# Performance work log

Hardware: AMD Instinct MI355X
Metric: run time of the kernel (lower is better)

The kernel has to match this reference:

```python
import jax, jax.numpy as jnp
import numpy as np

D = 128; H = 4; DK = D // H; ZN = 64; V = 8

def _silu(x):
    return x * jax.nn.sigmoid(x)

def _mlp3(x, w1, b1, w2, b2, w3, b3):
    h = _silu(x @ w1 + b1)
    h = _silu(h @ w2 + b2)
    return h @ w3 + b3

def _snorm(x):
    # StaticLayerNorm: center, divide by unbiased std (torch .std default ddof=1)
    c = x - jnp.mean(x, axis=-1, keepdims=True)
    std = jnp.sqrt(jnp.sum(c * c, axis=-1, keepdims=True) / (x.shape[-1] - 1))
    std = jnp.where(std == 0, 1.0, std)
    return c / std

def setup_inputs():
    key = jax.random.key(0)
    ks = list(jax.random.split(key, 40)); ki = iter(ks)
    xs = (6.0 / (DK + D)) ** 0.5
    inp = {}
    inp["latent"] = jax.random.normal(next(ki), (ZN, D, V, V, V), jnp.float32)
    inp["nodes"] = jax.random.normal(next(ki), (ZN, D), jnp.float32)
    inp["t"] = jax.random.uniform(next(ki), (ZN,), jnp.float32)
    for nm in ("qw", "kw", "vw"):
        inp[nm] = jax.random.uniform(next(ki), (H, D, DK), jnp.float32, -xs, xs)
    for nm in ("qb", "kb", "vb"):
        inp[nm] = jnp.zeros((H, DK), jnp.float32)
    inp["ow"] = jax.random.normal(next(ki), (D, D), jnp.float32) * (1.0 / D) ** 0.5
    for pre, dout in (("an_gb", 2 * D), ("an_a", D), ("fn_gb", 2 * D), ("fn_a", D)):
        inp[pre + "_w1"] = jax.random.normal(next(ki), (D, D), jnp.float32) * 0.05
        inp[pre + "_b1"] = jnp.zeros((D,), jnp.float32)
        inp[pre + "_w2"] = jax.random.normal(next(ki), (D, D), jnp.float32) * 0.05
        inp[pre + "_b2"] = jnp.zeros((D,), jnp.float32)
        inp[pre + "_w3"] = jax.random.normal(next(ki), (D, dout), jnp.float32) * 0.05
        inp[pre + "_b3"] = jnp.zeros((dout,), jnp.float32)
    return inp

def reference(latent, nodes, t, qw, kw, vw, qb, kb, vb, ow,
              an_gb_w1, an_gb_b1, an_gb_w2, an_gb_b2, an_gb_w3, an_gb_b3,
              an_a_w1, an_a_b1, an_a_w2, an_a_b2, an_a_w3, an_a_b3,
              fn_gb_w1, fn_gb_b1, fn_gb_w2, fn_gb_b2, fn_gb_w3, fn_gb_b3,
              fn_a_w1, fn_a_b1, fn_a_w2, fn_a_b2, fn_a_w3, fn_a_b3):
    b, d, vx, vy, vz = latent.shape
    n = vx * vy * vz
    x = latent.reshape(b, d, n).transpose(0, 2, 1)  # [b, n, d]
    cond = nodes[:, None, :] + t[:, None, None]     # [b, 1, d]
    gb1 = _mlp3(cond, an_gb_w1, an_gb_b1, an_gb_w2, an_gb_b2, an_gb_w3, an_gb_b3)
    g1, be1 = jnp.split(gb1, 2, axis=-1)
    al1 = _mlp3(cond, an_a_w1, an_a_b1, an_a_w2, an_a_b2, an_a_w3, an_a_b3)
    gb2 = _mlp3(cond, fn_gb_w1, fn_gb_b1, fn_gb_w2, fn_gb_b2, fn_gb_w3, fn_gb_b3)
    g2, be2 = jnp.split(gb2, 2, axis=-1)
    al2 = _mlp3(cond, fn_a_w1, fn_a_b1, fn_a_w2, fn_a_b2, fn_a_w3, fn_a_b3)
    # FAITHFUL BUG REPRO: source unpacks adaLN's (gamma, beta, alpha) as (alpha, gamma, beta)
    alpha1, gamma1, beta1 = g1, be1, al1
    alpha2, gamma2, beta2 = g2, be2, al2
    x2 = gamma1 * _snorm(x) + beta1
    dk = d // qw.shape[0]
    Q = jnp.einsum('bnd,hdk->bhnk', x2, qw) + qb[None, :, None, :]
    K = jnp.einsum('bnd,hdk->bhnk', x2, kw) + kb[None, :, None, :]
    Vv = jnp.einsum('bnd,hdk->bhnk', x2, vw) + vb[None, :, None, :]
    S = jnp.einsum('bhnk,bhmk->bhnm', Q, K) / (dk ** 0.5)
    P = jax.nn.softmax(S, axis=-1)
    O = jnp.einsum('bhnm,bhmk->bhnk', P, Vv)
    O = O.transpose(0, 2, 3, 1).reshape(b, n, d)  # matches torch permute(0,2,3,1).reshape
    attn = O @ ow
    x = x + alpha1 * attn
    x2 = gamma2 * _snorm(x) + beta2
    x = x + alpha2 * x2  # NOTE: source forward never applies self.ffn (dead module)
    return x.transpose(0, 2, 1).reshape(b, d, vx, vy, vz)
```

## Files before the change

### kernel.cpp

```cpp
#include <hip/hip_runtime.h>
#include <hip/hip_bf16.h>
#include <math.h>


#define NB 64

typedef __attribute__((ext_vector_type(8))) short bf16x8;
typedef __attribute__((ext_vector_type(4))) float f32x4;

__device__ __forceinline__ float silu_f(float x) { return x / (1.0f + __expf(-x)); }
__device__ __forceinline__ unsigned short f2bf(float x) {
    __hip_bfloat16 h = __float2bfloat16(x);
    return *reinterpret_cast<unsigned short*>(&h);
}

__global__ void __launch_bounds__(256) k_prep(
    const float* __restrict__ qw, const float* __restrict__ kw,
    const float* __restrict__ vw, const float* __restrict__ ow,
    unsigned short* __restrict__ cT, unsigned short* __restrict__ owT)
{
    int idx = blockIdx.x*256 + threadIdx.x;
    if (idx < 49152) {
        int ph = idx >> 14, r = idx & 16383, c = r >> 7, d = r & 127;
        int h = c >> 5, kk = c & 31;
        const float* wp = ph==0 ? qw : (ph==1 ? kw : vw);
        cT[idx] = f2bf(wp[h*4096 + d*32 + kk]);
    } else {
        int r = idx - 49152, c = r >> 7, i = r & 127;
        owT[r] = f2bf(ow[i*128 + c]);
    }
}

__global__ void __launch_bounds__(128) k_cond(
    const float* __restrict__ nodes, const float* __restrict__ tv,
    const float* __restrict__ w10, const float* __restrict__ b10,
    const float* __restrict__ w20, const float* __restrict__ b20,
    const float* __restrict__ w30, const float* __restrict__ b30,
    const float* __restrict__ w11, const float* __restrict__ b11,
    const float* __restrict__ w21, const float* __restrict__ b21,
    const float* __restrict__ w31, const float* __restrict__ b31,
    const float* __restrict__ w12, const float* __restrict__ b12,
    const float* __restrict__ w22, const float* __restrict__ b22,
    const float* __restrict__ w32, const float* __restrict__ b32,
    const float* __restrict__ w13, const float* __restrict__ b13,
    const float* __restrict__ w23, const float* __restrict__ b23,
    const float* __restrict__ w33, const float* __restrict__ b33,
    float* __restrict__ mods)
{
    int blk = blockIdx.x;
    int b = blk >> 2, m = blk & 3;
    const float* W1 = m==0?w10 : m==1?w11 : m==2?w12 : w13;
    const float* B1 = m==0?b10 : m==1?b11 : m==2?b12 : b13;
    const float* W2 = m==0?w20 : m==1?w21 : m==2?w22 : w23;
    const float* B2 = m==0?b20 : m==1?b21 : m==2?b22 : b23;
    const float* W3 = m==0?w30 : m==1?w31 : m==2?w32 : w33;
    const float* B3 = m==0?b30 : m==1?b31 : m==2?b32 : b33;
    int dout256 = (m == 0 || m == 2);
    int slot = (m==0)?0 : (m==1)?2 : (m==2)?3 : 5;

    __shared__ float xs[128], h1[128], h2[128];
    int t = threadIdx.x;
    xs[t] = nodes[b*128 + t] + tv[b];
    __syncthreads();

    float acc = B1[t];
    for (int i = 0; i < 128; i++) acc += xs[i] * W1[i*128 + t];
    h1[t] = silu_f(acc);
    __syncthreads();

    acc = B2[t];
    for (int i = 0; i < 128; i++) acc += h1[i] * W2[i*128 + t];
    h2[t] = silu_f(acc);
    __syncthreads();

    if (dout256) {
        float a0 = B3[t], a1 = B3[t + 128];
        for (int i = 0; i < 128; i++) {
            float h = h2[i];
            a0 += h * W3[i*256 + t];
            a1 += h * W3[i*256 + t + 128];
        }
        mods[((size_t)b*6 + slot    )*128 + t] = a0;
        mods[((size_t)b*6 + slot + 1)*128 + t] = a1;
    } else {
        float a0 = B3[t];
        for (int i = 0; i < 128; i++) a0 += h2[i] * W3[i*128 + t];
        mods[((size_t)b*6 + slot)*128 + t] = a0;
    }
}

__global__ void __launch_bounds__(256, 4) k_norm_qkv(
    const float* __restrict__ latent, const float* __restrict__ mods,
    const unsigned short* __restrict__ cT,
    const float* __restrict__ qb, const float* __restrict__ kb, const float* __restrict__ vb,
    unsigned short* __restrict__ Qb, unsigned short* __restrict__ Kb,
    unsigned short* __restrict__ Vtb)
{
    __shared__ unsigned short xb[64*136];

    int blk = blockIdx.x;
    int b = blk >> 3, n0 = (blk & 7) * 64;
    int t = threadIdx.x;
    int j = t >> 2, sub = t & 3;

    const float* lp = latent + (size_t)b*65536 + n0 + j;
    float lat[32];
    #pragma unroll
    for (int i = 0; i < 32; i++)
        lat[i] = lp[(size_t)(sub*32 + i)*512];

    float s = 0.f, ss = 0.f;
    #pragma unroll
    for (int i = 0; i < 32; i++) { s += lat[i]; ss += lat[i]*lat[i]; }
    s += __shfl_xor(s, 1); ss += __shfl_xor(ss, 1);
    s += __shfl_xor(s, 2); ss += __shfl_xor(ss, 2);
    float mean = s * (1.0f/128.0f);
    float var = (ss - 128.0f*mean*mean) * (1.0f/127.0f);
    var = var < 0.f ? 0.f : var;
    float sd = sqrtf(var);
    float rstd = (sd == 0.f) ? 1.f : 1.f/sd;

    const float* g1p  = mods + ((size_t)b*6 + 1)*128 + sub*32;
    const float* be1p = mods + ((size_t)b*6 + 2)*128 + sub*32;
    unsigned int* xbw = (unsigned int*)xb + j*68 + sub*16;
    #pragma unroll
    for (int i2 = 0; i2 < 16; i2++) {
        float v0 = g1p[2*i2]   * ((lat[2*i2]   - mean)*rstd) + be1p[2*i2];
        float v1 = g1p[2*i2+1] * ((lat[2*i2+1] - mean)*rstd) + be1p[2*i2+1];
        xbw[i2] = (unsigned)f2bf(v0) | ((unsigned)f2bf(v1) << 16);
    }
    __syncthreads();

    int w = t >> 6, lane = t & 63, lo = lane & 15, hi = lane >> 4;
    bf16x8 af[4];
    #pragma unroll
    for (int kc = 0; kc < 4; kc++)
        af[kc] = *(const bf16x8*)(xb + (w*16 + lo)*136 + kc*32 + hi*8);
    __syncthreads();

    const f32x4 zero = {0.f, 0.f, 0.f, 0.f};
    const float qscale = 0.17677669529663687f * 1.4426950408889634f;

    #pragma unroll 1
    for (int ph = 0; ph < 3; ph++) {
        const unsigned short* ct = cT + ph*16384;
        for (int nt = 0; nt < 8; nt++) {
            f32x4 acc = zero;
            #pragma unroll
            for (int kc = 0; kc < 4; kc++) {
                bf16x8 bf = *(const bf16x8*)(ct + (nt*16 + lo)*128 + kc*32 + hi*8);
                acc = __builtin_amdgcn_mfma_f32_16x16x32_bf16(af[kc], bf, acc, 0, 0, 0);
            }
            int c = nt*16 + lo, h = c >> 5, kk = c & 31;
            size_t bh = (size_t)(b*4 + h);
            if (ph == 0) {
                float bias = qb[c];
                #pragma unroll
                for (int jj = 0; jj < 4; jj++) {
                    int n = n0 + w*16 + hi*4 + jj;
                    Qb[(bh*512 + n)*32 + kk] = f2bf((acc[jj] + bias) * qscale);
                }
            } else if (ph == 1) {
                float bias = kb[c];
                #pragma unroll
                for (int jj = 0; jj < 4; jj++) {
                    int n = n0 + w*16 + hi*4 + jj;
                    Kb[(bh*512 + n)*32 + kk] = f2bf(acc[jj] + bias);
                }
            } else {
                float bias = vb[c];
                #pragma unroll
                for (int jj = 0; jj < 4; jj++) {
                    int nl = w*16 + hi*4 + jj;
                    xb[c*68 + nl] = f2bf(acc[jj] + bias);
                }
            }
        }
    }
    __syncthreads();
    for (int idx = t; idx < 8192; idx += 256) {
        int c = idx >> 6, jj = idx & 63;
        int h = c >> 5, kk = c & 31;
        size_t bh = (size_t)(b*4 + h);
        Vtb[(bh*32 + kk)*512 + n0 + jj] = xb[c*68 + jj];
    }
}

__global__ void __launch_bounds__(512, 4) k_attn(
    const unsigned short* __restrict__ Qb, const unsigned short* __restrict__ Kb,
    const unsigned short* __restrict__ Vtb, unsigned short* __restrict__ Ob)
{
    __shared__ unsigned short KsS[512*32];
    __shared__ unsigned short VsS[32*512];

    int blk = blockIdx.x;
    int bh = blk >> 1, qhalf = blk & 1;
    int t = threadIdx.x;

    const unsigned short* kgp = Kb + (size_t)bh*512*32;
    const unsigned short* vgp = Vtb + (size_t)bh*32*512;
    for (int idx = t; idx < 2048; idx += 512)
        *(bf16x8*)(KsS + idx*8) = *(const bf16x8*)(kgp + idx*8);
    for (int idx = t; idx < 2048; idx += 512) {
        int r = idx >> 6, cch = idx & 63;
        *(bf16x8*)(VsS + r*512 + ((cch*8) ^ ((r&7)<<3))) =
            *(const bf16x8*)(vgp + r*512 + cch*8);
    }
    __syncthreads();

    int w = t >> 6, lane = t & 63, lo = lane & 15, hi = lane >> 4;
    const unsigned short* qbase = Qb + (size_t)bh*512*32;
    const f32x4 zero = {0.f, 0.f, 0.f, 0.f};
    int b = bh >> 2, h = bh & 3;

    const unsigned short* Vl0 = VsS + lo*512;
    const unsigned short* Vl1 = VsS + (16 + lo)*512;
    int swz = (lo & 7) << 3;
    int srcA = lo + 32*(hi & 1);

    for (int qt = 0; qt < 2; ++qt) {
        int q0 = qhalf*256 + w*32 + qt*16;
        bf16x8 qa = *(const bf16x8*)(qbase + (size_t)(q0 + lo)*32 + hi*8);

        float m = -1e30f, sum = 0.f;
        f32x4 oa = zero, ob = zero;

        #pragma unroll 1
        for (int ch = 0; ch < 4; ++ch) {
            f32x4 s8[8];
            #pragma unroll
            for (int kt = 0; kt < 8; ++kt) {
                bf16x8 kf = *(const bf16x8*)(KsS + ((ch*8 + kt)*16 + lo)*32 + hi*8);
                s8[kt] = __builtin_amdgcn_mfma_f32_16x16x32_bf16(kf, qa, zero, 0, 0, 0);
            }

            float cm = -1e30f;
            #pragma unroll
            for (int kt = 0; kt < 8; ++kt)
                cm = fmaxf(cm, fmaxf(fmaxf(s8[kt][0], s8[kt][1]), fmaxf(s8[kt][2], s8[kt][3])));
            cm = fmaxf(cm, __shfl_xor(cm, 16));
            cm = fmaxf(cm, __shfl_xor(cm, 32));
            float nm = fmaxf(m, cm);
            float sc = __builtin_amdgcn_exp2f(m - nm);
            sum *= sc;
            #pragma unroll
            for (int jj = 0; jj < 4; ++jj) { oa[jj] *= sc; ob[jj] *= sc; }
            m = nm;

            unsigned pw0c[8], pw1c[8];
            #pragma unroll
            for (int kt = 0; kt < 8; ++kt) {
                float p0 = __builtin_amdgcn_exp2f(s8[kt][0] - nm);
                float p1 = __builtin_amdgcn_exp2f(s8[kt][1] - nm);
                float p2 = __builtin_amdgcn_exp2f(s8[kt][2] - nm);
                float p3 = __builtin_amdgcn_exp2f(s8[kt][3] - nm);
                sum += (p0 + p1) + (p2 + p3);
                pw0c[kt] = (unsigned)f2bf(p0) | ((unsigned)f2bf(p1) << 16);
                pw1c[kt] = (unsigned)f2bf(p2) | ((unsigned)f2bf(p3) << 16);
            }

            #pragma unroll
            for (int kt2 = 0; kt2 < 4; ++kt2) {
                unsigned e0 = pw0c[2*kt2],     e1 = pw1c[2*kt2];
                unsigned o0 = pw0c[2*kt2 + 1], o1 = pw1c[2*kt2 + 1];
                unsigned ae0 = (unsigned)__shfl((int)e0, srcA, 64);
                unsigned ae1 = (unsigned)__shfl((int)e1, srcA, 64);
                unsigned ao0 = (unsigned)__shfl((int)o0, srcA, 64);
                unsigned ao1 = (unsigned)__shfl((int)o1, srcA, 64);
                unsigned be0 = (unsigned)__shfl((int)e0, srcA + 16, 64);
                unsigned be1 = (unsigned)__shfl((int)e1, srcA + 16, 64);
                unsigned bo0 = (unsigned)__shfl((int)o0, srcA + 16, 64);
                unsigned bo1 = (unsigned)__shfl((int)o1, srcA + 16, 64);
                union { unsigned u[4]; bf16x8 v; } pb;
                pb.u[0] = (hi < 2) ? ae0 : ao0;
                pb.u[1] = (hi < 2) ? ae1 : ao1;
                pb.u[2] = (hi < 2) ? be0 : bo0;
                pb.u[3] = (hi < 2) ? be1 : bo1;
                int off = (((ch*4 + kt2)*32) + hi*8) ^ swz;
                bf16x8 v0 = *(const bf16x8*)(Vl0 + off);
                bf16x8 v1 = *(const bf16x8*)(Vl1 + off);
                oa = __builtin_amdgcn_mfma_f32_16x16x32_bf16(v0, pb.v, oa, 0, 0, 0);
                ob = __builtin_amdgcn_mfma_f32_16x16x32_bf16(v1, pb.v, ob, 0, 0, 0);
            }
        }

        sum += __shfl_xor(sum, 16);
        sum += __shfl_xor(sum, 32);

        float inv = 1.f / sum;
        unsigned short* op = Ob + ((size_t)(b*512 + q0 + lo))*128 + h;
        #pragma unroll
        for (int jj = 0; jj < 4; ++jj) {
            op[(hi*4 + jj)*4]       = f2bf(oa[jj] * inv);
            op[(16 + hi*4 + jj)*4]  = f2bf(ob[jj] * inv);
        }
    }
}

__global__ void __launch_bounds__(256, 4) k_out(
    const float* __restrict__ latent, const unsigned short* __restrict__ Ob,
    const unsigned short* __restrict__ owT, const float* __restrict__ mods,
    float* __restrict__ outp)
{
    __shared__ float xs[64*129];
    __shared__ float a1s[128], a2s[128], g2s[128], b2s[128];
    __shared__ float mean_s[64], rstd_s[64];

    int blk = blockIdx.x;
    int b = blk >> 3, n0 = (blk & 7) * 64;
    int t = threadIdx.x;

    if (t < 128) {
        a1s[t] = mods[((size_t)b*6 + 0)*128 + t];
        a2s[t] = mods[((size_t)b*6 + 3)*128 + t];
        g2s[t] = mods[((size_t)b*6 + 4)*128 + t];
        b2s[t] = mods[((size_t)b*6 + 5)*128 + t];
    }
    const float* lp = latent + (size_t)b*65536 + n0;
    for (int idx = t; idx < 8192; idx += 256) {
        int d = idx >> 6, jj = idx & 63;
        xs[jj*129 + d] = lp[(size_t)d*512 + jj];
    }
    __syncthreads();

    int w = t >> 6, lane = t & 63, lo = lane & 15, hi = lane >> 4;

    const unsigned short* arow = Ob + ((size_t)(b*512 + n0 + w*16 + lo))*128;
    bf16x8 af[4];
    #pragma unroll
    for (int kc = 0; kc < 4; kc++)
        af[kc] = *(const bf16x8*)(arow + kc*32 + hi*8);

    const f32x4 zero = {0.f, 0.f, 0.f, 0.f};
    for (int nt = 0; nt < 8; nt++) {
        f32x4 acc = zero;
        #pragma unroll
        for (int kc = 0; kc < 4; kc++) {
            bf16x8 bf = *(const bf16x8*)(owT + (nt*16 + lo)*128 + kc*32 + hi*8);
            acc = __builtin_amdgcn_mfma_f32_16x16x32_bf16(af[kc], bf, acc, 0, 0, 0);
        }
        int c = nt*16 + lo;
        #pragma unroll
        for (int jj = 0; jj < 4; jj++) {
            int nl = w*16 + hi*4 + jj;
            xs[nl*129 + c] += a1s[c] * acc[jj];
        }
    }
    __syncthreads();

    {
        int row = t >> 2, sub = t & 3;
        float s = 0.f, ss = 0.f;
        const float* xr = &xs[row*129 + sub*32];
        #pragma unroll
        for (int i = 0; i < 32; i++) { float v = xr[i]; s += v; ss += v*v; }
        s += __shfl_xor(s, 1); ss += __shfl_xor(ss, 1);
        s += __shfl_xor(s, 2); ss += __shfl_xor(ss, 2);
        float mean = s * (1.0f/128.0f);
        float var = (ss - 128.0f*mean*mean) * (1.0f/127.0f);
        var = var < 0.f ? 0.f : var;
        float sd = sqrtf(var);
        mean_s[row] = mean;
        rstd_s[row] = (sd == 0.f) ? 1.f : 1.f/sd;
    }
    __syncthreads();

    float* outb = outp + (size_t)b*65536 + n0;
    for (int idx = t; idx < 8192; idx += 256) {
        int d = idx >> 6, jj = idx & 63;
        float v = xs[jj*129 + d];
        float nv = (v - mean_s[jj]) * rstd_s[jj];
        outb[(size_t)d*512 + jj] = v + a2s[d]*(g2s[d]*nv + b2s[d]);
    }
}

extern "C" void kernel_launch(void* const* d_in, const int* in_sizes, int n_in,
                              void* d_out, int out_size, void* d_ws, size_t ws_size,
                              hipStream_t stream) {
    const float* latent = (const float*)d_in[0];
    const float* nodes  = (const float*)d_in[1];
    const float* tv     = (const float*)d_in[2];
    const float* qw     = (const float*)d_in[3];
    const float* kw     = (const float*)d_in[4];
    const float* vw     = (const float*)d_in[5];
    const float* qb     = (const float*)d_in[6];
    const float* kb     = (const float*)d_in[7];
    const float* vb     = (const float*)d_in[8];
    const float* owp    = (const float*)d_in[9];

    const float* mw[24];
    for (int i = 0; i < 24; i++) mw[i] = (const float*)d_in[10 + i];

    char* wsb = (char*)d_ws;
    unsigned short* Qb  = (unsigned short*)(wsb);
    unsigned short* Kb  = (unsigned short*)(wsb + 8388608);
    unsigned short* Vtb = (unsigned short*)(wsb + 16777216);
    unsigned short* Ob  = (unsigned short*)(wsb + 25165824);
    float* mods         = (float*)(wsb + 33554432);
    unsigned short* cT  = (unsigned short*)(wsb + 33751040);
    unsigned short* owT = (unsigned short*)(wsb + 33849344);

    float* outp = (float*)d_out;

    k_prep<<<dim3(256), dim3(256), 0, stream>>>(qw, kw, vw, owp, cT, owT);

    k_cond<<<dim3(NB*4), dim3(128), 0, stream>>>(
        nodes, tv,
        mw[0], mw[1], mw[2], mw[3], mw[4], mw[5],
        mw[6], mw[7], mw[8], mw[9], mw[10], mw[11],
        mw[12], mw[13], mw[14], mw[15], mw[16], mw[17],
        mw[18], mw[19], mw[20], mw[21], mw[22], mw[23],
        mods);

    k_norm_qkv<<<dim3(NB*8), dim3(256), 0, stream>>>(
        latent, mods, cT, qb, kb, vb, Qb, Kb, Vtb);

    k_attn<<<dim3(NB*4*2), dim3(512), 0, stream>>>(Qb, Kb, Vtb, Ob);

    k_out<<<dim3(NB*8), dim3(256), 0, stream>>>(latent, Ob, owT, mods, outp);
}
```

Baseline: 226.2 us.

## Fuse weight prep into cond kernel and stage GEMM weights in LDS

The separate weight-conversion kernel is merged into the conditioning MLP kernel as extra blocks, which removes one launch. The QKV and output-projection kernels now copy each bf16 weight matrix into padded shared memory before the MFMA loop, instead of reading the B fragments straight from global memory. This cuts repeated global/L2 traffic for the weights. The cost is more LDS per block, so the launch-bounds occupancy hints are lowered, and the QKV kernel adds extra barriers around each phase.

```diff
diff --git a/kernel.cpp b/kernel.cpp
--- a/kernel.cpp
+++ b/kernel.cpp
@@ -12,23 +12,6 @@
 __device__ __forceinline__ unsigned short f2bf(float x) {
     __hip_bfloat16 h = __float2bfloat16(x);
     return *reinterpret_cast<unsigned short*>(&h);
-}
-
-__global__ void __launch_bounds__(256) k_prep(
-    const float* __restrict__ qw, const float* __restrict__ kw,
-    const float* __restrict__ vw, const float* __restrict__ ow,
-    unsigned short* __restrict__ cT, unsigned short* __restrict__ owT)
-{
-    int idx = blockIdx.x*256 + threadIdx.x;
-    if (idx < 49152) {
-        int ph = idx >> 14, r = idx & 16383, c = r >> 7, d = r & 127;
-        int h = c >> 5, kk = c & 31;
-        const float* wp = ph==0 ? qw : (ph==1 ? kw : vw);
-        cT[idx] = f2bf(wp[h*4096 + d*32 + kk]);
-    } else {
-        int r = idx - 49152, c = r >> 7, i = r & 127;
-        owT[r] = f2bf(ow[i*128 + c]);
-    }
 }
 
 __global__ void __launch_bounds__(128) k_cond(
@@ -45,9 +28,32 @@
     const float* __restrict__ w13, const float* __restrict__ b13,
     const float* __restrict__ w23, const float* __restrict__ b23,
     const float* __restrict__ w33, const float* __restrict__ b33,
-    float* __restrict__ mods)
+    float* __restrict__ mods,
+    const float* __restrict__ qw, const float* __restrict__ kw,
+    const float* __restrict__ vw, const float* __restrict__ ow,
+    unsigned short* __restrict__ cT, unsigned short* __restrict__ owT)
 {
     int blk = blockIdx.x;
+    int t = threadIdx.x;
+
+    if (blk >= NB*4) {
+        int pbase = (blk - NB*4)*128 + t;
+        #pragma unroll
+        for (int rep = 0; rep < 2; rep++) {
+            int idx = pbase + rep*32768;
+            if (idx < 49152) {
+                int ph = idx >> 14, r = idx & 16383, c = r >> 7, d = r & 127;
+                int h = c >> 5, kk = c & 31;
+                const float* wp = ph==0 ? qw : (ph==1 ? kw : vw);
+                cT[idx] = f2bf(wp[h*4096 + d*32 + kk]);
+            } else {
+                int r = idx - 49152, c = r >> 7, i = r & 127;
+                owT[r] = f2bf(ow[i*128 + c]);
+            }
+        }
+        return;
+    }
+
     int b = blk >> 2, m = blk & 3;
     const float* W1 = m==0?w10 : m==1?w11 : m==2?w12 : w13;
     const float* B1 = m==0?b10 : m==1?b11 : m==2?b12 : b13;
@@ -59,7 +65,6 @@
     int slot = (m==0)?0 : (m==1)?2 : (m==2)?3 : 5;
 
     __shared__ float xs[128], h1[128], h2[128];
-    int t = threadIdx.x;
     xs[t] = nodes[b*128 + t] + tv[b];
     __syncthreads();
 
@@ -89,7 +94,7 @@
     }
 }
 
-__global__ void __launch_bounds__(256, 4) k_norm_qkv(
+__global__ void __launch_bounds__(256, 3) k_norm_qkv(
     const float* __restrict__ latent, const float* __restrict__ mods,
     const unsigned short* __restrict__ cT,
     const float* __restrict__ qb, const float* __restrict__ kb, const float* __restrict__ vb,
@@ -97,6 +102,7 @@
     unsigned short* __restrict__ Vtb)
 {
     __shared__ unsigned short xb[64*136];
+    __shared__ unsigned short WtS[128*136];
 
     int blk = blockIdx.x;
     int b = blk >> 3, n0 = (blk & 7) * 64;
@@ -136,19 +142,31 @@
     #pragma unroll
     for (int kc = 0; kc < 4; kc++)
         af[kc] = *(const bf16x8*)(xb + (w*16 + lo)*136 + kc*32 + hi*8);
-    __syncthreads();
 
     const f32x4 zero = {0.f, 0.f, 0.f, 0.f};
     const float qscale = 0.17677669529663687f * 1.4426950408889634f;
+    unsigned int* WtSw = (unsigned int*)WtS;
 
     #pragma unroll 1
     for (int ph = 0; ph < 3; ph++) {
-        const unsigned short* ct = cT + ph*16384;
+        __syncthreads();
+        {
+            const uint4* cq = (const uint4*)(cT + ph*16384);
+            #pragma unroll
+            for (int k = 0; k < 8; k++) {
+                int idx4 = t + k*256;
+                int c = idx4 >> 4, d2b = (idx4 & 15)*4;
+                uint4 v = cq[idx4];
+                *(uint4*)(WtSw + c*68 + d2b) = v;
+            }
+        }
+        __syncthreads();
+
         for (int nt = 0; nt < 8; nt++) {
             f32x4 acc = zero;
             #pragma unroll
             for (int kc = 0; kc < 4; kc++) {
-                bf16x8 bf = *(const bf16x8*)(ct + (nt*16 + lo)*128 + kc*32 + hi*8);
+                bf16x8 bf = *(const bf16x8*)(WtS + (nt*16 + lo)*136 + kc*32 + hi*8);
                 acc = __builtin_amdgcn_mfma_f32_16x16x32_bf16(af[kc], bf, acc, 0, 0, 0);
             }
             int c = nt*16 + lo, h = c >> 5, kk = c & 31;
@@ -297,11 +315,12 @@
     }
 }
 
-__global__ void __launch_bounds__(256, 4) k_out(
+__global__ void __launch_bounds__(256, 2) k_out(
     const float* __restrict__ latent, const unsigned short* __restrict__ Ob,
     const unsigned short* __restrict__ owT, const float* __restrict__ mods,
     float* __restrict__ outp)
 {
+    __shared__ unsigned short owS[128*136];
     __shared__ float xs[64*129];
     __shared__ float a1s[128], a2s[128], g2s[128], b2s[128];
     __shared__ float mean_s[64], rstd_s[64];
@@ -316,6 +335,17 @@
         g2s[t] = mods[((size_t)b*6 + 4)*128 + t];
         b2s[t] = mods[((size_t)b*6 + 5)*128 + t];
     }
+    {
+        unsigned int* owSw = (unsigned int*)owS;
+        const uint4* oq = (const uint4*)owT;
+        #pragma unroll
+        for (int k = 0; k < 8; k++) {
+            int idx4 = t + k*256;
+            int c = idx4 >> 4, d2b = (idx4 & 15)*4;
+            uint4 v = oq[idx4];
+            *(uint4*)(owSw + c*68 + d2b) = v;
+        }
+    }
     const float* lp = latent + (size_t)b*65536 + n0;
     for (int idx = t; idx < 8192; idx += 256) {
         int d = idx >> 6, jj = idx & 63;
@@ -336,7 +366,7 @@
         f32x4 acc = zero;
         #pragma unroll
         for (int kc = 0; kc < 4; kc++) {
-            bf16x8 bf = *(const bf16x8*)(owT + (nt*16 + lo)*128 + kc*32 + hi*8);
+            bf16x8 bf = *(const bf16x8*)(owS + (nt*16 + lo)*136 + kc*32 + hi*8);
             acc = __builtin_amdgcn_mfma_f32_16x16x32_bf16(af[kc], bf, acc, 0, 0, 0);
         }
         int c = nt*16 + lo;
@@ -402,15 +432,14 @@
 
     float* outp = (float*)d_out;
 
-    k_prep<<<dim3(256), dim3(256), 0, stream>>>(qw, kw, vw, owp, cT, owT);
-
-    k_cond<<<dim3(NB*4), dim3(128), 0, stream>>>(
+    k_cond<<<dim3(NB*4 + 256), dim3(128), 0, stream>>>(
         nodes, tv,
         mw[0], mw[1], mw[2], mw[3], mw[4], mw[5],
         mw[6], mw[7], mw[8], mw[9], mw[10], mw[11],
         mw[12], mw[13], mw[14], mw[15], mw[16], mw[17],
         mw[18], mw[19], mw[20], mw[21], mw[22], mw[23],
-        mods);
+        mods,
+        qw, kw, vw, owp, cT, owT);
 
     k_norm_qkv<<<dim3(NB*8), dim3(256), 0, stream>>>(
         latent, mods, cT, qb, kb, vb, Qb, Kb, Vtb);
```

After: 200.8 us. 1.13x faster.
